# Performance work log

Measured on AMD Instinct MI355X. Metric: run time of the kernel, lower is better.

Reference implementation:

```python
import jax, jax.numpy as jnp
import numpy as np


def gcn_conv(x, edge_index, edge_weight, W, b):
    """PyG-style GCNConv: h = x @ W; add self-loops (w=1); sym deg^-1/2 norm;
    scatter-add aggregation; + bias."""
    N = x.shape[0]
    h = x @ W                                   # [N, F_out]
    row, col = edge_index[0], edge_index[1]     # src, dst
    loop = jnp.arange(N)
    row = jnp.concatenate([row, loop])
    col = jnp.concatenate([col, loop])
    ew = jnp.concatenate([edge_weight, jnp.ones((N,), edge_weight.dtype)])
    deg = jax.ops.segment_sum(ew, col, num_segments=N)
    dinv = jnp.where(deg > 0, deg ** -0.5, 0.0)
    norm = dinv[row] * ew * dinv[col]           # [E+N]
    out = jax.ops.segment_sum(h[row] * norm[:, None], col, num_segments=N)
    return out + b


def setup_inputs() -> dict:
    key = jax.random.key(0)
    ks = jax.random.split(key, 12)
    N, F_in, H, O, E = 20000, 3000, 512, 256, 640000
    x = jax.random.normal(ks[0], (N, F_in), dtype=jnp.float32)
    sim_edge_index = jax.random.randint(ks[1], (2, E), 0, N, dtype=jnp.int64)
    sim_edge_weight = jax.random.uniform(ks[2], (E,), dtype=jnp.float32)
    dist_edge_index = jax.random.randint(ks[3], (2, E), 0, N, dtype=jnp.int64)
    dist_edge_weight = jax.random.uniform(ks[4], (E,), dtype=jnp.float32)
    s = 0.02
    return {
        "x": x,
        "sim_edge_index": sim_edge_index,
        "sim_edge_weight": sim_edge_weight,
        "dist_edge_index": dist_edge_index,
        "dist_edge_weight": dist_edge_weight,
        "W1": jax.random.normal(ks[5], (F_in, H), dtype=jnp.float32) * s,
        "b1": jnp.zeros((H,), jnp.float32),
        "W2": jax.random.normal(ks[6], (F_in, H), dtype=jnp.float32) * s,
        "b2": jnp.zeros((H,), jnp.float32),
        "Ws": jax.random.normal(ks[7], (H, O), dtype=jnp.float32) * s,
        "bs": jnp.zeros((O,), jnp.float32),
        "Wd": jax.random.normal(ks[8], (H, O), dtype=jnp.float32) * s,
        "bd": jnp.zeros((O,), jnp.float32),
        "Wf": jax.random.normal(ks[9], (2 * O, O), dtype=jnp.float32) * s,
        "bf": jnp.zeros((O,), jnp.float32),
    }


def reference(x, sim_edge_index, sim_edge_weight, dist_edge_index,
              dist_edge_weight, W1, b1, W2, b2, Ws, bs, Wd, bd, Wf, bf):
    # eval mode: dropout is identity
    xs = jax.nn.relu(gcn_conv(x, sim_edge_index, sim_edge_weight, W1, b1))
    xd = jax.nn.relu(gcn_conv(x, dist_edge_index, dist_edge_weight, W2, b2))
    x_sim = gcn_conv(xs, sim_edge_index, sim_edge_weight, Ws, bs)
    x_dist = gcn_conv(xd, dist_edge_index, dist_edge_weight, Wd, bd)
    fused = jnp.concatenate([x_sim, x_dist], axis=1) @ Wf + bf
    return (x_sim, x_dist, fused)
```

## Files before the change

### kernel.cpp

```cpp
#include <hip/hip_runtime.h>
#include <cstdint>
#include <cstddef>

typedef unsigned short u16;
typedef __bf16 bf16x8 __attribute__((ext_vector_type(8)));
typedef float f32x4 __attribute__((ext_vector_type(4)));

#define N_NODES 20000
#define MPAD    20096
#define E_EDGES 640000
#define K1      3000
#define K1P     3008
#define H_DIM   512
#define NW      1024
#define O_DIM   256

__device__ __forceinline__ float bf2f(unsigned int hi) {
  union { unsigned int u; float f; } v; v.u = hi << 16; return v.f;
}
__device__ __forceinline__ u16 f2bf(float f) {
  union { float f; unsigned int u; } v; v.f = f;
  unsigned int u = v.u;
  return (u16)((u + 0x7fffu + ((u >> 16) & 1u)) >> 16);
}

__device__ __forceinline__ void gl2lds16(const void* g, void* l) {
  __builtin_amdgcn_global_load_lds((const __attribute__((address_space(1))) void*)g,
                                   (__attribute__((address_space(3))) void*)l, 16, 0, 0);
}

__global__ __launch_bounds__(256) void deg_init_k(float* degS, float* degD, int* cntS, int* cntD) {
  int i = blockIdx.x * 256 + threadIdx.x;
  if (i < N_NODES) { degS[i] = 1.0f; degD[i] = 1.0f; cntS[i] = 0; cntD[i] = 0; }
}

__global__ __launch_bounds__(256) void deg_accum_k(const int* eiS, const float* ewS,
                                                   const int* eiD, const float* ewD,
                                                   float* degS, float* degD, int* cntS, int* cntD,
                                                   int* eposS, int* eposD) {
  int e = blockIdx.x * 256 + threadIdx.x;
  if (e < E_EDGES) {
    int cs = eiS[E_EDGES + e];
    atomicAdd(&degS[cs], ewS[e]);
    eposS[e] = atomicAdd(&cntS[cs], 1);
    int cd = eiD[E_EDGES + e];
    atomicAdd(&degD[cd], ewD[e]);
    eposD[e] = atomicAdd(&cntD[cd], 1);
  }
}

__global__ __launch_bounds__(1024) void scan_k(const int* cntS, int* offS,
                                               const float* degS, float* dinvS,
                                               const int* cntD, int* offD,
                                               const float* degD, float* dinvD) {
  extern __shared__ int lds[];
  int* sums = lds;
  int* lcnt = lds + 1024;
  const int* cnt = blockIdx.x ? cntD : cntS;
  int* off = blockIdx.x ? offD : offS;
  const float* deg = blockIdx.x ? degD : degS;
  float* dinv = blockIdx.x ? dinvD : dinvS;
  const int t = threadIdx.x;

  for (int idx = t; idx < N_NODES; idx += 1024) {
    lcnt[idx] = cnt[idx];
    dinv[idx] = rsqrtf(deg[idx]);
  }
  __syncthreads();

  const int CH = 20;
  const int base = t * CH;
  int s = 0;
#pragma unroll
  for (int j = 0; j < CH; ++j) { int idx = base + j; if (idx < N_NODES) s += lcnt[idx]; }
  sums[t] = s;
  __syncthreads();
  for (int d = 1; d < 1024; d <<= 1) {
    int v = (t >= d) ? sums[t - d] : 0;
    __syncthreads();
    sums[t] += v;
    __syncthreads();
  }
  int run = sums[t] - s;
#pragma unroll
  for (int j = 0; j < CH; ++j) {
    int idx = base + j;
    if (idx < N_NODES) { int c = lcnt[idx]; lcnt[idx] = run; run += c; }
  }
  __syncthreads();
  for (int idx = t; idx < N_NODES; idx += 1024) off[idx] = lcnt[idx];
  if (t == 1023) off[N_NODES] = run;
}

__global__ __launch_bounds__(256) void scatter_k(const int* eiS, const float* ewS, const float* dinvS,
                                                 const int* offS, const int* eposS,
                                                 int* ssrcS, float* snrmS,
                                                 const int* eiD, const float* ewD, const float* dinvD,
                                                 const int* offD, const int* eposD,
                                                 int* ssrcD, float* snrmD) {
  int e = blockIdx.x * 256 + threadIdx.x;
  if (e < E_EDGES) {
    {
      int r = eiS[e], c = eiS[E_EDGES + e];
      int pos = offS[c] + eposS[e];
      ssrcS[pos] = r;
      snrmS[pos] = dinvS[r] * ewS[e] * dinvS[c];
    }
    {
      int r = eiD[e], c = eiD[E_EDGES + e];
      int pos = offD[c] + eposD[e];
      ssrcD[pos] = r;
      snrmD[pos] = dinvD[r] * ewD[e] * dinvD[c];
    }
  }
}

__global__ __launch_bounds__(256) void conv_x_k(const float* __restrict__ x, u16* __restrict__ xb) {
  const int row = blockIdx.x;
  for (int c = threadIdx.x; c < 376; c += 256) {
    uint4 o = {0, 0, 0, 0};
    if (row < N_NODES && c < 375) {
      const float4* p = (const float4*)(x + (size_t)row * K1 + (size_t)c * 8);
      float4 v0 = p[0], v1 = p[1];
      o.x = f2bf(v0.x) | ((unsigned)f2bf(v0.y) << 16);
      o.y = f2bf(v0.z) | ((unsigned)f2bf(v0.w) << 16);
      o.z = f2bf(v1.x) | ((unsigned)f2bf(v1.y) << 16);
      o.w = f2bf(v1.z) | ((unsigned)f2bf(v1.w) << 16);
    }
    *(uint4*)(xb + (size_t)row * K1P + (size_t)c * 8) = o;
  }
}

__global__ __launch_bounds__(256) void conv_w12_k(const float* __restrict__ W1,
                                                  const float* __restrict__ W2,
                                                  u16* __restrict__ w12t) {
  __shared__ float t[64][65];
  const int kb = blockIdx.x;
  const int nb = blockIdx.y;
  const int n0 = nb * 64;
  const float* W = (n0 < H_DIM) ? W1 : W2;
  const int nn0 = n0 & (H_DIM - 1);
  const int k0 = kb * 64;
  const int tc = threadIdx.x & 63;
  const int tr4 = threadIdx.x >> 6;
#pragma unroll
  for (int rr = 0; rr < 16; ++rr) {
    int r = tr4 * 16 + rr;
    int k = k0 + r;
    t[r][tc] = (k < K1) ? W[(size_t)k * H_DIM + nn0 + tc] : 0.f;
  }
  __syncthreads();
#pragma unroll
  for (int rr = 0; rr < 16; ++rr) {
    int n = tr4 * 16 + rr;
    w12t[(size_t)(n0 + n) * K1P + k0 + tc] = f2bf(t[tc][n]);
  }
}

__global__ __launch_bounds__(256) void conv_wsm_k(const float* Ws, const float* Wd, const float* Wf,
                                                  u16* wst, u16* wdt, u16* wft) {
  __shared__ float t[64][65];
  const int which = blockIdx.z;
  const float* W = (which == 0) ? Ws : (which == 1) ? Wd : Wf;
  u16* o = (which == 0) ? wst : (which == 1) ? wdt : wft;
  const int k0 = blockIdx.x * 64;
  const int n0 = blockIdx.y * 64;
  const int tc = threadIdx.x & 63;
  const int tr4 = threadIdx.x >> 6;
#pragma unroll
  for (int rr = 0; rr < 16; ++rr) {
    int r = tr4 * 16 + rr;
    t[r][tc] = W[(size_t)(k0 + r) * O_DIM + n0 + tc];
  }
  __syncthreads();
#pragma unroll
  for (int rr = 0; rr < 16; ++rr) {
    int n = tr4 * 16 + rr;
    o[(size_t)(n0 + n) * H_DIM + k0 + tc] = f2bf(t[tc][n]);
  }
}

template <typename CT, bool BIAS>
__device__ __forceinline__ void gemm_body(const u16* __restrict__ A, const u16* __restrict__ Bt,
                                          CT* __restrict__ C, const float* __restrict__ bias,
                                          int Mreal, int K, int ldc, int bm, int bn) {
  __shared__ alignas(16) u16 As[128 * 64];
  __shared__ alignas(16) u16 Bs[128 * 64];
  const int tid = threadIdx.x;
  const int lane = tid & 63;
  const int wv = tid >> 6;

  const int wm = (wv >> 1) << 6;
  const int wn = (wv & 1) << 6;
  const int frow = lane & 15;
  const int q = lane >> 4;
  const int r7 = lane & 7;

  const int srow = tid >> 3;
  const int sgr = ((tid & 7) ^ ((tid >> 3) & 7)) << 3;
  const u16* ga = A + (size_t)(bm + srow) * K + sgr;
  const u16* gb = Bt + (size_t)(bn + srow) * K + sgr;
  u16* la = &As[wv * 512];
  u16* lb = &Bs[wv * 512];

  f32x4 acc[4][4] = {};

  for (int k0 = 0; k0 < K; k0 += 64) {
#pragma unroll
    for (int r = 0; r < 4; ++r) {
      gl2lds16(ga + (size_t)(r * 32) * K + k0, la + r * 2048);
      gl2lds16(gb + (size_t)(r * 32) * K + k0, lb + r * 2048);
    }
    __syncthreads();
#pragma unroll
    for (int ks = 0; ks < 64; ks += 32) {
      const int p = (((q + (ks >> 3)) ^ r7) << 3);
      bf16x8 af[4], bv[4];
#pragma unroll
      for (int t = 0; t < 4; ++t) {
        af[t] = *(const bf16x8*)&As[(wm + t * 16 + frow) * 64 + p];
        bv[t] = *(const bf16x8*)&Bs[(wn + t * 16 + frow) * 64 + p];
      }
#pragma unroll
      for (int i = 0; i < 4; ++i)
#pragma unroll
        for (int j = 0; j < 4; ++j)
          acc[i][j] = __builtin_amdgcn_mfma_f32_16x16x32_bf16(af[i], bv[j], acc[i][j], 0, 0, 0);
    }
    __syncthreads();
  }

  const int crow = (lane >> 4) << 2;
  const int ccol = lane & 15;
#pragma unroll
  for (int i = 0; i < 4; ++i) {
#pragma unroll
    for (int r = 0; r < 4; ++r) {
      int gr = bm + wm + i * 16 + crow + r;
      if (gr < Mreal) {
#pragma unroll
        for (int j = 0; j < 4; ++j) {
          int gc = bn + wn + j * 16 + ccol;
          float v = acc[i][j][r];
          if constexpr (BIAS) v += bias[gc];
          if constexpr (sizeof(CT) == 2) C[(size_t)gr * ldc + gc] = (CT)f2bf(v);
          else C[(size_t)gr * ldc + gc] = (CT)v;
        }
      }
    }
  }
}

__global__ __launch_bounds__(256) void gemm_big_k(const u16* __restrict__ A,
                                                  const u16* __restrict__ Bt,
                                                  u16* __restrict__ C) {
  const int h = blockIdx.y * 8 + blockIdx.x;
  const int chunk = 157;
  const int L = (h & 7) * chunk + (h >> 3);
  const int bn = (L & 7) * 128;
  const int bm = (L >> 3) * 128;
  gemm_body<u16, false>(A, Bt, C, nullptr, N_NODES, K1P, NW, bm, bn);
}

__global__ __launch_bounds__(256) void gemm_pair_k(const u16* A0, const u16* B0, u16* C0,
                                                   const u16* A1, const u16* B1, u16* C1) {
  const u16* A = blockIdx.z ? A1 : A0;
  const u16* Bt = blockIdx.z ? B1 : B0;
  u16* C = blockIdx.z ? C1 : C0;
  gemm_body<u16, false>(A, Bt, C, nullptr, N_NODES, H_DIM, O_DIM,
                        blockIdx.y * 128, blockIdx.x * 128);
}

__global__ __launch_bounds__(256) void gemm_f_k(const u16* A, const u16* Bt, float* C,
                                                const float* bias) {
  gemm_body<float, true>(A, Bt, C, bias, N_NODES, H_DIM, O_DIM,
                         blockIdx.y * 128, blockIdx.x * 128);
}

__global__ __launch_bounds__(256) void agg1_k(const u16* __restrict__ h12,
                                              const int* offS, const int* srcS, const float* nrmS,
                                              const float* dinvS, const float* b1,
                                              const int* offD, const int* srcD, const float* nrmD,
                                              const float* dinvD, const float* b2,
                                              u16* __restrict__ xsd) {
  const int lane = threadIdx.x & 63;
  const int wv = threadIdx.x >> 6;
  const int i = blockIdx.x * 4 + wv;
  const int g = blockIdx.y;
  if (i >= MPAD) return;
  u16* outp = xsd + ((size_t)g * MPAD + i) * H_DIM + lane * 8;
  if (i >= N_NODES) { uint4 z = {0, 0, 0, 0}; *(uint4*)outp = z; return; }

  const int* off = g ? offD : offS;
  const int* src = g ? srcD : srcS;
  const float* nrm = g ? nrmD : nrmS;
  const float* dinv = g ? dinvD : dinvS;
  const float* bias = g ? b2 : b1;
  const u16* hb = h12 + (size_t)g * H_DIM + lane * 8;

  float a[8];
  float dv = dinv[i];
  float sw = dv * dv;
  uint4 u = *(const uint4*)(hb + (size_t)i * NW);
  a[0] = sw * bf2f(u.x & 0xffff); a[1] = sw * bf2f(u.x >> 16);
  a[2] = sw * bf2f(u.y & 0xffff); a[3] = sw * bf2f(u.y >> 16);
  a[4] = sw * bf2f(u.z & 0xffff); a[5] = sw * bf2f(u.z >> 16);
  a[6] = sw * bf2f(u.w & 0xffff); a[7] = sw * bf2f(u.w >> 16);

  const int e0 = off[i], e1 = off[i + 1];
  int e = e0;
  for (; e + 6 <= e1; e += 6) {
    int ss[6]; float ww[6];
#pragma unroll
    for (int t = 0; t < 6; ++t) { ss[t] = src[e + t]; ww[t] = nrm[e + t]; }
    uint4 vv[6];
#pragma unroll
    for (int t = 0; t < 6; ++t) vv[t] = *(const uint4*)(hb + (size_t)ss[t] * NW);
#pragma unroll
    for (int t = 0; t < 6; ++t) {
      float w = ww[t]; uint4 v = vv[t];
      a[0] += w * bf2f(v.x & 0xffff); a[1] += w * bf2f(v.x >> 16);
      a[2] += w * bf2f(v.y & 0xffff); a[3] += w * bf2f(v.y >> 16);
      a[4] += w * bf2f(v.z & 0xffff); a[5] += w * bf2f(v.z >> 16);
      a[6] += w * bf2f(v.w & 0xffff); a[7] += w * bf2f(v.w >> 16);
    }
  }
  for (; e < e1; ++e) {
    int s = src[e];
    float w = nrm[e];
    uint4 v = *(const uint4*)(hb + (size_t)s * NW);
    a[0] += w * bf2f(v.x & 0xffff); a[1] += w * bf2f(v.x >> 16);
    a[2] += w * bf2f(v.y & 0xffff); a[3] += w * bf2f(v.y >> 16);
    a[4] += w * bf2f(v.z & 0xffff); a[5] += w * bf2f(v.z >> 16);
    a[6] += w * bf2f(v.w & 0xffff); a[7] += w * bf2f(v.w >> 16);
  }
  float4 bA = *(const float4*)(bias + lane * 8);
  float4 bB = *(const float4*)(bias + lane * 8 + 4);
  a[0] = fmaxf(a[0] + bA.x, 0.f); a[1] = fmaxf(a[1] + bA.y, 0.f);
  a[2] = fmaxf(a[2] + bA.z, 0.f); a[3] = fmaxf(a[3] + bA.w, 0.f);
  a[4] = fmaxf(a[4] + bB.x, 0.f); a[5] = fmaxf(a[5] + bB.y, 0.f);
  a[6] = fmaxf(a[6] + bB.z, 0.f); a[7] = fmaxf(a[7] + bB.w, 0.f);
  uint4 o;
  o.x = f2bf(a[0]) | ((unsigned)f2bf(a[1]) << 16);
  o.y = f2bf(a[2]) | ((unsigned)f2bf(a[3]) << 16);
  o.z = f2bf(a[4]) | ((unsigned)f2bf(a[5]) << 16);
  o.w = f2bf(a[6]) | ((unsigned)f2bf(a[7]) << 16);
  *(uint4*)outp = o;
}

__global__ __launch_bounds__(256) void agg2_k(const u16* __restrict__ hsb, const u16* __restrict__ hdb,
                                              const int* offS, const int* srcS, const float* nrmS,
                                              const float* dinvS, const float* bs,
                                              const int* offD, const int* srcD, const float* nrmD,
                                              const float* dinvD, const float* bd,
                                              float* __restrict__ outF, u16* __restrict__ xcat) {
  const int lane = threadIdx.x & 63;
  const int wv = threadIdx.x >> 6;
  const int i = blockIdx.x * 4 + wv;
  const int g = blockIdx.y;
  if (i >= MPAD) return;
  u16* oc = xcat + (size_t)i * H_DIM + (size_t)g * O_DIM + lane * 4;
  if (i >= N_NODES) { uint2 z = {0, 0}; *(uint2*)oc = z; return; }

  const u16* h = g ? hdb : hsb;
  const int* off = g ? offD : offS;
  const int* src = g ? srcD : srcS;
  const float* nrm = g ? nrmD : nrmS;
  const float* dinv = g ? dinvD : dinvS;
  const float* bias = g ? bd : bs;
  const u16* hb = h + lane * 4;

  float a[4];
  float dv = dinv[i];
  float sw = dv * dv;
  uint2 u = *(const uint2*)(hb + (size_t)i * O_DIM);
  a[0] = sw * bf2f(u.x & 0xffff); a[1] = sw * bf2f(u.x >> 16);
  a[2] = sw * bf2f(u.y & 0xffff); a[3] = sw * bf2f(u.y >> 16);

  const int e0 = off[i], e1 = off[i + 1];
  int e = e0;
  for (; e + 8 <= e1; e += 8) {
    int ss[8]; float ww[8];
#pragma unroll
    for (int t = 0; t < 8; ++t) { ss[t] = src[e + t]; ww[t] = nrm[e + t]; }
    uint2 vv[8];
#pragma unroll
    for (int t = 0; t < 8; ++t) vv[t] = *(const uint2*)(hb + (size_t)ss[t] * O_DIM);
#pragma unroll
    for (int t = 0; t < 8; ++t) {
      float w = ww[t]; uint2 v = vv[t];
      a[0] += w * bf2f(v.x & 0xffff); a[1] += w * bf2f(v.x >> 16);
      a[2] += w * bf2f(v.y & 0xffff); a[3] += w * bf2f(v.y >> 16);
    }
  }
  for (; e < e1; ++e) {
    int s = src[e];
    float w = nrm[e];
    uint2 v = *(const uint2*)(hb + (size_t)s * O_DIM);
    a[0] += w * bf2f(v.x & 0xffff); a[1] += w * bf2f(v.x >> 16);
    a[2] += w * bf2f(v.y & 0xffff); a[3] += w * bf2f(v.y >> 16);
  }
  float4 bb = *(const float4*)(bias + lane * 4);
  a[0] += bb.x; a[1] += bb.y; a[2] += bb.z; a[3] += bb.w;

  float4 fo = {a[0], a[1], a[2], a[3]};
  *(float4*)(outF + (size_t)g * N_NODES * O_DIM + (size_t)i * O_DIM + lane * 4) = fo;
  uint2 o;
  o.x = f2bf(a[0]) | ((unsigned)f2bf(a[1]) << 16);
  o.y = f2bf(a[2]) | ((unsigned)f2bf(a[3]) << 16);
  *(uint2*)oc = o;
}

extern "C" void kernel_launch(void* const* d_in, const int* in_sizes, int n_in,
                              void* d_out, int out_size, void* d_ws, size_t ws_size,
                              hipStream_t stream) {
  const float* x = (const float*)d_in[0];
  const int* eiS = (const int*)d_in[1];
  const float* ewS = (const float*)d_in[2];
  const int* eiD = (const int*)d_in[3];
  const float* ewD = (const float*)d_in[4];
  const float* W1 = (const float*)d_in[5];
  const float* b1 = (const float*)d_in[6];
  const float* W2 = (const float*)d_in[7];
  const float* b2 = (const float*)d_in[8];
  const float* Ws = (const float*)d_in[9];
  const float* bs = (const float*)d_in[10];
  const float* Wd = (const float*)d_in[11];
  const float* bd = (const float*)d_in[12];
  const float* Wf = (const float*)d_in[13];
  const float* bf_ = (const float*)d_in[14];
  float* out = (float*)d_out;

  char* p = (char*)d_ws;
  auto alloc = [&](size_t n) -> char* { char* r = p; p += (n + 255) & ~(size_t)255; return r; };

  u16* xb    = (u16*)alloc((size_t)MPAD * K1P * 2);
  u16* w12t  = (u16*)alloc((size_t)NW * K1P * 2);
  u16* h12   = (u16*)alloc((size_t)N_NODES * NW * 2);
  u16* xsd   = (u16*)alloc((size_t)2 * MPAD * H_DIM * 2);
  u16* hsb   = (u16*)alloc((size_t)N_NODES * O_DIM * 2);
  u16* hdb   = (u16*)alloc((size_t)N_NODES * O_DIM * 2);
  u16* xcat  = (u16*)alloc((size_t)MPAD * H_DIM * 2);
  u16* wst   = (u16*)alloc((size_t)O_DIM * H_DIM * 2);
  u16* wdt   = (u16*)alloc((size_t)O_DIM * H_DIM * 2);
  u16* wft   = (u16*)alloc((size_t)O_DIM * H_DIM * 2);
  float* degS = (float*)alloc((size_t)N_NODES * 4);
  float* degD = (float*)alloc((size_t)N_NODES * 4);
  float* dinvS = (float*)alloc((size_t)N_NODES * 4);
  float* dinvD = (float*)alloc((size_t)N_NODES * 4);
  int* cntS = (int*)alloc((size_t)N_NODES * 4);
  int* cntD = (int*)alloc((size_t)N_NODES * 4);
  int* offS = (int*)alloc((size_t)(N_NODES + 1) * 4);
  int* offD = (int*)alloc((size_t)(N_NODES + 1) * 4);
  int* eposS = (int*)alloc((size_t)E_EDGES * 4);
  int* eposD = (int*)alloc((size_t)E_EDGES * 4);
  int* ssrcS = (int*)alloc((size_t)E_EDGES * 4);
  int* ssrcD = (int*)alloc((size_t)E_EDGES * 4);
  float* snrmS = (float*)alloc((size_t)E_EDGES * 4);
  float* snrmD = (float*)alloc((size_t)E_EDGES * 4);

  const int gN = (N_NODES + 255) / 256;
  const int gE = (E_EDGES + 255) / 256;

  deg_init_k<<<gN, 256, 0, stream>>>(degS, degD, cntS, cntD);
  deg_accum_k<<<gE, 256, 0, stream>>>(eiS, ewS, eiD, ewD, degS, degD, cntS, cntD, eposS, eposD);
  scan_k<<<2, 1024, (size_t)(1024 + N_NODES) * 4, stream>>>(cntS, offS, degS, dinvS,
                                                            cntD, offD, degD, dinvD);
  scatter_k<<<gE, 256, 0, stream>>>(eiS, ewS, dinvS, offS, eposS, ssrcS, snrmS,
                                    eiD, ewD, dinvD, offD, eposD, ssrcD, snrmD);

  conv_x_k<<<MPAD, 256, 0, stream>>>(x, xb);
  conv_w12_k<<<dim3(47, 16), 256, 0, stream>>>(W1, W2, w12t);
  conv_wsm_k<<<dim3(8, 4, 3), 256, 0, stream>>>(Ws, Wd, Wf, wst, wdt, wft);

  gemm_big_k<<<dim3(8, 157), 256, 0, stream>>>(xb, w12t, h12);

  agg1_k<<<dim3(MPAD / 4, 2), 256, 0, stream>>>(h12, offS, ssrcS, snrmS, dinvS, b1,
                                                offD, ssrcD, snrmD, dinvD, b2, xsd);

  gemm_pair_k<<<dim3(2, 157, 2), 256, 0, stream>>>(xsd, wst, hsb,
                                                   xsd + (size_t)MPAD * H_DIM, wdt, hdb);

  agg2_k<<<dim3(MPAD / 4, 2), 256, 0, stream>>>(hsb, hdb, offS, ssrcS, snrmS, dinvS, bs,
                                                offD, ssrcD, snrmD, dinvD, bd, out, xcat);

  gemm_f_k<<<dim3(2, 157), 256, 0, stream>>>(xcat, wft, out + (size_t)2 * N_NODES * O_DIM, bf_);
}
```

Before: 1.022 ms.

## Merge preprocessing kernels and overlap edge scatter with big GEMM

Merges the x/weight bf16 conversions and the degree-accumulation pass into one multi-role kernel, and folds the CSR scatter into the big GEMM launch as extra trailing blocks. The aim is to cut launch count and let independent, latency-bound edge work run alongside compute-bound GEMM tiles instead of serializing. The cost is that the merged kernels reserve the 64x65 float shared tile and the GEMM's shared memory for every block, and the branchy role dispatch may lower occupancy for the lightweight edge blocks.

```diff
diff --git a/kernel.cpp b/kernel.cpp
--- a/kernel.cpp
+++ b/kernel.cpp
@@ -15,6 +15,9 @@
 #define NW      1024
 #define O_DIM   256
 
+#define NB_GEMM   1256
+#define NB_EDGE   2500
+
 __device__ __forceinline__ float bf2f(unsigned int hi) {
   union { unsigned int u; float f; } v; v.u = hi << 16; return v.f;
 }
@@ -34,18 +37,95 @@
   if (i < N_NODES) { degS[i] = 1.0f; degD[i] = 1.0f; cntS[i] = 0; cntD[i] = 0; }
 }
 
-__global__ __launch_bounds__(256) void deg_accum_k(const int* eiS, const float* ewS,
-                                                   const int* eiD, const float* ewD,
-                                                   float* degS, float* degD, int* cntS, int* cntD,
-                                                   int* eposS, int* eposD) {
-  int e = blockIdx.x * 256 + threadIdx.x;
-  if (e < E_EDGES) {
-    int cs = eiS[E_EDGES + e];
-    atomicAdd(&degS[cs], ewS[e]);
-    eposS[e] = atomicAdd(&cntS[cs], 1);
-    int cd = eiD[E_EDGES + e];
-    atomicAdd(&degD[cd], ewD[e]);
-    eposD[e] = atomicAdd(&cntD[cd], 1);
+__global__ __launch_bounds__(256) void pre_k(const float* __restrict__ x, u16* __restrict__ xb,
+                                             const float* __restrict__ W1, const float* __restrict__ W2,
+                                             u16* __restrict__ w12t,
+                                             const float* Ws, const float* Wd, const float* Wf,
+                                             u16* wst, u16* wdt, u16* wft,
+                                             const int* eiS, const float* ewS,
+                                             const int* eiD, const float* ewD,
+                                             float* degS, float* degD, int* cntS, int* cntD,
+                                             int* eposS, int* eposD) {
+  __shared__ float t[64][65];
+  int b = blockIdx.x;
+
+  if (b < MPAD) {
+    const int row = b;
+    for (int c = threadIdx.x; c < 376; c += 256) {
+      uint4 o = {0, 0, 0, 0};
+      if (row < N_NODES && c < 375) {
+        const float4* p = (const float4*)(x + (size_t)row * K1 + (size_t)c * 8);
+        float4 v0 = p[0], v1 = p[1];
+        o.x = f2bf(v0.x) | ((unsigned)f2bf(v0.y) << 16);
+        o.y = f2bf(v0.z) | ((unsigned)f2bf(v0.w) << 16);
+        o.z = f2bf(v1.x) | ((unsigned)f2bf(v1.y) << 16);
+        o.w = f2bf(v1.z) | ((unsigned)f2bf(v1.w) << 16);
+      }
+      *(uint4*)(xb + (size_t)row * K1P + (size_t)c * 8) = o;
+    }
+    return;
+  }
+  b -= MPAD;
+
+  if (b < 752) {
+    const int kb = b % 47;
+    const int nb = b / 47;
+    const int n0 = nb * 64;
+    const float* W = (n0 < H_DIM) ? W1 : W2;
+    const int nn0 = n0 & (H_DIM - 1);
+    const int k0 = kb * 64;
+    const int tc = threadIdx.x & 63;
+    const int tr4 = threadIdx.x >> 6;
+#pragma unroll
+    for (int rr = 0; rr < 16; ++rr) {
+      int r = tr4 * 16 + rr;
+      int k = k0 + r;
+      t[r][tc] = (k < K1) ? W[(size_t)k * H_DIM + nn0 + tc] : 0.f;
+    }
+    __syncthreads();
+#pragma unroll
+    for (int rr = 0; rr < 16; ++rr) {
+      int n = tr4 * 16 + rr;
+      w12t[(size_t)(n0 + n) * K1P + k0 + tc] = f2bf(t[tc][n]);
+    }
+    return;
+  }
+  b -= 752;
+
+  if (b < 96) {
+    const int which = b >> 5;
+    const int rem = b & 31;
+    const float* W = (which == 0) ? Ws : (which == 1) ? Wd : Wf;
+    u16* o = (which == 0) ? wst : (which == 1) ? wdt : wft;
+    const int k0 = (rem & 7) * 64;
+    const int n0 = (rem >> 3) * 64;
+    const int tc = threadIdx.x & 63;
+    const int tr4 = threadIdx.x >> 6;
+#pragma unroll
+    for (int rr = 0; rr < 16; ++rr) {
+      int r = tr4 * 16 + rr;
+      t[r][tc] = W[(size_t)(k0 + r) * O_DIM + n0 + tc];
+    }
+    __syncthreads();
+#pragma unroll
+    for (int rr = 0; rr < 16; ++rr) {
+      int n = tr4 * 16 + rr;
+      o[(size_t)(n0 + n) * H_DIM + k0 + tc] = f2bf(t[tc][n]);
+    }
+    return;
+  }
+  b -= 96;
+
+  {
+    int e = b * 256 + threadIdx.x;
+    if (e < E_EDGES) {
+      int cs = eiS[E_EDGES + e];
+      atomicAdd(&degS[cs], ewS[e]);
+      eposS[e] = atomicAdd(&cntS[cs], 1);
+      int cd = eiD[E_EDGES + e];
+      atomicAdd(&degD[cd], ewD[e]);
+      eposD[e] = atomicAdd(&cntD[cd], 1);
+    }
   }
 }
 
@@ -92,94 +172,6 @@
   if (t == 1023) off[N_NODES] = run;
 }
 
-__global__ __launch_bounds__(256) void scatter_k(const int* eiS, const float* ewS, const float* dinvS,
-                                                 const int* offS, const int* eposS,
-                                                 int* ssrcS, float* snrmS,
-                                                 const int* eiD, const float* ewD, const float* dinvD,
-                                                 const int* offD, const int* eposD,
-                                                 int* ssrcD, float* snrmD) {
-  int e = blockIdx.x * 256 + threadIdx.x;
-  if (e < E_EDGES) {
-    {
-      int r = eiS[e], c = eiS[E_EDGES + e];
-      int pos = offS[c] + eposS[e];
-      ssrcS[pos] = r;
-      snrmS[pos] = dinvS[r] * ewS[e] * dinvS[c];
-    }
-    {
-      int r = eiD[e], c = eiD[E_EDGES + e];
-      int pos = offD[c] + eposD[e];
-      ssrcD[pos] = r;
-      snrmD[pos] = dinvD[r] * ewD[e] * dinvD[c];
-    }
-  }
-}
-
-__global__ __launch_bounds__(256) void conv_x_k(const float* __restrict__ x, u16* __restrict__ xb) {
-  const int row = blockIdx.x;
-  for (int c = threadIdx.x; c < 376; c += 256) {
-    uint4 o = {0, 0, 0, 0};
-    if (row < N_NODES && c < 375) {
-      const float4* p = (const float4*)(x + (size_t)row * K1 + (size_t)c * 8);
-      float4 v0 = p[0], v1 = p[1];
-      o.x = f2bf(v0.x) | ((unsigned)f2bf(v0.y) << 16);
-      o.y = f2bf(v0.z) | ((unsigned)f2bf(v0.w) << 16);
-      o.z = f2bf(v1.x) | ((unsigned)f2bf(v1.y) << 16);
-      o.w = f2bf(v1.z) | ((unsigned)f2bf(v1.w) << 16);
-    }
-    *(uint4*)(xb + (size_t)row * K1P + (size_t)c * 8) = o;
-  }
-}
-
-__global__ __launch_bounds__(256) void conv_w12_k(const float* __restrict__ W1,
-                                                  const float* __restrict__ W2,
-                                                  u16* __restrict__ w12t) {
-  __shared__ float t[64][65];
-  const int kb = blockIdx.x;
-  const int nb = blockIdx.y;
-  const int n0 = nb * 64;
-  const float* W = (n0 < H_DIM) ? W1 : W2;
-  const int nn0 = n0 & (H_DIM - 1);
-  const int k0 = kb * 64;
-  const int tc = threadIdx.x & 63;
-  const int tr4 = threadIdx.x >> 6;
-#pragma unroll
-  for (int rr = 0; rr < 16; ++rr) {
-    int r = tr4 * 16 + rr;
-    int k = k0 + r;
-    t[r][tc] = (k < K1) ? W[(size_t)k * H_DIM + nn0 + tc] : 0.f;
-  }
-  __syncthreads();
-#pragma unroll
-  for (int rr = 0; rr < 16; ++rr) {
-    int n = tr4 * 16 + rr;
-    w12t[(size_t)(n0 + n) * K1P + k0 + tc] = f2bf(t[tc][n]);
-  }
-}
-
-__global__ __launch_bounds__(256) void conv_wsm_k(const float* Ws, const float* Wd, const float* Wf,
-                                                  u16* wst, u16* wdt, u16* wft) {
-  __shared__ float t[64][65];
-  const int which = blockIdx.z;
-  const float* W = (which == 0) ? Ws : (which == 1) ? Wd : Wf;
-  u16* o = (which == 0) ? wst : (which == 1) ? wdt : wft;
-  const int k0 = blockIdx.x * 64;
-  const int n0 = blockIdx.y * 64;
-  const int tc = threadIdx.x & 63;
-  const int tr4 = threadIdx.x >> 6;
-#pragma unroll
-  for (int rr = 0; rr < 16; ++rr) {
-    int r = tr4 * 16 + rr;
-    t[r][tc] = W[(size_t)(k0 + r) * O_DIM + n0 + tc];
-  }
-  __syncthreads();
-#pragma unroll
-  for (int rr = 0; rr < 16; ++rr) {
-    int n = tr4 * 16 + rr;
-    o[(size_t)(n0 + n) * H_DIM + k0 + tc] = f2bf(t[tc][n]);
-  }
-}
-
 template <typename CT, bool BIAS>
 __device__ __forceinline__ void gemm_body(const u16* __restrict__ A, const u16* __restrict__ Bt,
                                           CT* __restrict__ C, const float* __restrict__ bias,
@@ -251,15 +243,38 @@
   }
 }
 
-__global__ __launch_bounds__(256) void gemm_big_k(const u16* __restrict__ A,
-                                                  const u16* __restrict__ Bt,
-                                                  u16* __restrict__ C) {
-  const int h = blockIdx.y * 8 + blockIdx.x;
-  const int chunk = 157;
-  const int L = (h & 7) * chunk + (h >> 3);
-  const int bn = (L & 7) * 128;
-  const int bm = (L >> 3) * 128;
-  gemm_body<u16, false>(A, Bt, C, nullptr, N_NODES, K1P, NW, bm, bn);
+__global__ __launch_bounds__(256) void gemm_sc_k(const u16* __restrict__ A,
+                                                 const u16* __restrict__ Bt,
+                                                 u16* __restrict__ C,
+                                                 const int* eiS, const float* ewS, const float* dinvS,
+                                                 const int* offS, const int* eposS,
+                                                 int* ssrcS, float* snrmS,
+                                                 const int* eiD, const float* ewD, const float* dinvD,
+                                                 const int* offD, const int* eposD,
+                                                 int* ssrcD, float* snrmD) {
+  int b = blockIdx.x;
+  if (b < NB_GEMM) {
+    const int chunk = 157;
+    const int L = (b & 7) * chunk + (b >> 3);
+    gemm_body<u16, false>(A, Bt, C, nullptr, N_NODES, K1P, NW, (L >> 3) * 128, (L & 7) * 128);
+    return;
+  }
+  b -= NB_GEMM;
+  int e = b * 256 + threadIdx.x;
+  if (e < E_EDGES) {
+    {
+      int r = eiS[e], c = eiS[E_EDGES + e];
+      int pos = offS[c] + eposS[e];
+      ssrcS[pos] = r;
+      snrmS[pos] = dinvS[r] * ewS[e] * dinvS[c];
+    }
+    {
+      int r = eiD[e], c = eiD[E_EDGES + e];
+      int pos = offD[c] + eposD[e];
+      ssrcD[pos] = r;
+      snrmD[pos] = dinvD[r] * ewD[e] * dinvD[c];
+    }
+  }
 }
 
 __global__ __launch_bounds__(256) void gemm_pair_k(const u16* A0, const u16* B0, u16* C0,
@@ -460,20 +475,20 @@
   float* snrmD = (float*)alloc((size_t)E_EDGES * 4);
 
   const int gN = (N_NODES + 255) / 256;
-  const int gE = (E_EDGES + 255) / 256;
 
   deg_init_k<<<gN, 256, 0, stream>>>(degS, degD, cntS, cntD);
-  deg_accum_k<<<gE, 256, 0, stream>>>(eiS, ewS, eiD, ewD, degS, degD, cntS, cntD, eposS, eposD);
+
+  pre_k<<<MPAD + 752 + 96 + NB_EDGE, 256, 0, stream>>>(
+      x, xb, W1, W2, w12t, Ws, Wd, Wf, wst, wdt, wft,
+      eiS, ewS, eiD, ewD, degS, degD, cntS, cntD, eposS, eposD);
+
   scan_k<<<2, 1024, (size_t)(1024 + N_NODES) * 4, stream>>>(cntS, offS, degS, dinvS,
                                                             cntD, offD, degD, dinvD);
-  scatter_k<<<gE, 256, 0, stream>>>(eiS, ewS, dinvS, offS, eposS, ssrcS, snrmS,
-                                    eiD, ewD, dinvD, offD, eposD, ssrcD, snrmD);
-
-  conv_x_k<<<MPAD, 256, 0, stream>>>(x, xb);
-  conv_w12_k<<<dim3(47, 16), 256, 0, stream>>>(W1, W2, w12t);
-  conv_wsm_k<<<dim3(8, 4, 3), 256, 0, stream>>>(Ws, Wd, Wf, wst, wdt, wft);
-
-  gemm_big_k<<<dim3(8, 157), 256, 0, stream>>>(xb, w12t, h12);
+
+  gemm_sc_k<<<NB_GEMM + NB_EDGE, 256, 0, stream>>>(
+      xb, w12t, h12,
+      eiS, ewS, dinvS, offS, eposS, ssrcS, snrmS,
+      eiD, ewD, dinvD, offD, eposD, ssrcD, snrmD);
 
   agg1_k<<<dim3(MPAD / 4, 2), 256, 0, stream>>>(h12, offS, ssrcS, snrmS, dinvS, b1,
                                                 offD, ssrcD, snrmD, dinvD, b2, xsd);
```

Result: faster. 988.2 us (-3.4%).
